# Kernel optimization log

Measured on AMD Instinct MI355X. Metric: run time of the kernel, lower is better.

## Reference

```python
import jax, jax.numpy as jnp
import numpy as np

K = 16  # matches init kwarg k


def setup_inputs() -> dict:
    key = jax.random.key(0)
    point_cloud = jax.random.normal(key, (4, 64, 4096), dtype=jnp.float32)
    return {"point_cloud": point_cloud}


def reference(point_cloud):
    B, dims, N = point_cloud.shape
    xt = jnp.transpose(point_cloud, (0, 2, 1))  # (B, N, dims)
    # pairwise euclidean distances (cdist, p=2)
    sq = jnp.sum(xt * xt, axis=-1)  # (B, N)
    d2 = sq[:, :, None] + sq[:, None, :] - 2.0 * jnp.einsum('bnd,bmd->bnm', xt, xt)
    dist = jnp.sqrt(jnp.maximum(d2, 0.0))  # (B, N, N)
    # k+1 smallest distances; drop self (first) neighbor
    _, idx_o = jax.lax.top_k(-dist, K + 1)  # (B, N, K+1)
    idx = idx_o[:, :, 1:]  # (B, N, K)
    # gather neighbor features: neighbors[b,d,n,j] = point_cloud[b,d,idx[b,n,j]]
    neighbors = jax.vmap(lambda pc, i: pc[:, i])(point_cloud, idx)  # (B, dims, N, K)
    central = point_cloud[:, :, :, None]  # (B, dims, N, 1)
    edge_feature = jnp.concatenate(
        [jnp.broadcast_to(central, (B, dims, N, K)), neighbors - central], axis=1
    )  # (B, 2*dims, N, K)
    return edge_feature, idx.reshape(B, -1)
```

## Files before the change

kernel.cpp:

```cpp
#include <hip/hip_runtime.h>


#define BATCH 4
#define DIMS 64
#define NPTS 4096
#define KNN 16
#define NCHUNK 32
#define CHLEN 128
#define GSZ 16
#define RN (BATCH * NPTS)
#define MLANES 8
#define MCH (NCHUNK / MLANES)

typedef unsigned long long u64;
typedef unsigned int u32;

__device__ __forceinline__ double sentinel() {
    return __longlong_as_double(0x7FEFFFFFFFFFFFFFLL);
}

__global__ __launch_bounds__(256) void ef_sq_kernel(const float* __restrict__ pc,
                                                    float* __restrict__ sq) {
    int gid = blockIdx.x * 256 + threadIdx.x;
    int b = gid >> 12;
    int n = gid & (NPTS - 1);
    const float* p = pc + (size_t)b * DIMS * NPTS + n;
    float r[8];
#pragma unroll
    for (int j = 0; j < 8; ++j) {
        float v = p[(size_t)j * NPTS];
        r[j] = __fmul_rn(v, v);
    }
#pragma unroll
    for (int i = 8; i < DIMS; i += 8) {
#pragma unroll
        for (int j = 0; j < 8; ++j) {
            float v = p[(size_t)(i + j) * NPTS];
            r[j] = __fadd_rn(r[j], __fmul_rn(v, v));
        }
    }
    float t01 = __fadd_rn(r[0], r[1]);
    float t23 = __fadd_rn(r[2], r[3]);
    float t45 = __fadd_rn(r[4], r[5]);
    float t67 = __fadd_rn(r[6], r[7]);
    sq[gid] = __fadd_rn(__fadd_rn(t01, t23), __fadd_rn(t45, t67));
}

__global__ __launch_bounds__(256) void ef_transpose(const float* __restrict__ pc,
                                                    float* __restrict__ pcT) {
    __shared__ float smT[DIMS][65];
    int tid = threadIdx.x;
    int m0 = blockIdx.x * 64;
    int b = blockIdx.y;
    const float* pcb = pc + (size_t)b * DIMS * NPTS;
#pragma unroll
    for (int i = 0; i < 16; ++i) {
        int idx = i * 256 + tid;
        int d = idx >> 6;
        int m = idx & 63;
        smT[d][m] = pcb[(size_t)d * NPTS + m0 + m];
    }
    __syncthreads();
#pragma unroll
    for (int i = 0; i < 16; ++i) {
        int idx = i * 256 + tid;
        int m = idx >> 6;
        int d = idx & 63;
        pcT[((size_t)b * NPTS + m0 + m) * DIMS + d] = smT[d][m];
    }
}

__global__ __launch_bounds__(256, 3) void ef_knn_partial(const float* __restrict__ pc,
                                                         const float* __restrict__ sq,
                                                         u64* __restrict__ pKey) {
    __shared__ float tile[DIMS][CHLEN];
    __shared__ float tileSq[CHLEN];
    int tid = threadIdx.x;
    int r = blockIdx.x * 256 + tid;
    int c = blockIdx.y;
    int b = (blockIdx.x * 256) >> 12;
    int n = r & (NPTS - 1);
    int m0 = c * CHLEN;
    const float* pcb = pc + (size_t)b * DIMS * NPTS;

    float xr[DIMS];
#pragma unroll
    for (int d = 0; d < DIMS; ++d) xr[d] = pcb[(size_t)d * NPTS + n];
#pragma unroll
    for (int d = 0; d < DIMS; ++d) asm volatile("" : "+v"(xr[d]));
    float sqn = sq[r];

#pragma unroll
    for (int i = 0; i < 8; ++i) {
        int idx = tid + i * 256;
        int d = idx >> 5;
        int mq = idx & 31;
        float4 v = *(const float4*)(pcb + (size_t)d * NPTS + m0 + mq * 4);
        *(float4*)&tile[d][mq * 4] = v;
    }
    if (tid < CHLEN / 4)
        *(float4*)&tileSq[tid * 4] =
            *(const float4*)(sq + (size_t)b * NPTS + m0 + tid * 4);
    __syncthreads();

    double key[KNN];
#pragma unroll
    for (int j = 0; j < KNN; ++j) key[j] = sentinel();

#define CE(arr, i, jj) { double lo_ = fmin(arr[i], arr[jj]); double hi_ = fmax(arr[i], arr[jj]); arr[i] = lo_; arr[jj] = hi_; }

    for (int g = 0; g < CHLEN; g += GSZ) {
        float acc[GSZ];
#pragma unroll
        for (int j = 0; j < GSZ; ++j) acc[j] = 0.f;
#pragma unroll
        for (int d = 0; d < DIMS; ++d) {
            float xv = xr[d];
            float4 q0 = *(const float4*)&tile[d][g];
            float4 q1 = *(const float4*)&tile[d][g + 4];
            float4 q2 = *(const float4*)&tile[d][g + 8];
            float4 q3 = *(const float4*)&tile[d][g + 12];
            acc[0]  = fmaf(xv, q0.x, acc[0]);
            acc[1]  = fmaf(xv, q0.y, acc[1]);
            acc[2]  = fmaf(xv, q0.z, acc[2]);
            acc[3]  = fmaf(xv, q0.w, acc[3]);
            acc[4]  = fmaf(xv, q1.x, acc[4]);
            acc[5]  = fmaf(xv, q1.y, acc[5]);
            acc[6]  = fmaf(xv, q1.z, acc[6]);
            acc[7]  = fmaf(xv, q1.w, acc[7]);
            acc[8]  = fmaf(xv, q2.x, acc[8]);
            acc[9]  = fmaf(xv, q2.y, acc[9]);
            acc[10] = fmaf(xv, q2.z, acc[10]);
            acc[11] = fmaf(xv, q2.w, acc[11]);
            acc[12] = fmaf(xv, q3.x, acc[12]);
            acc[13] = fmaf(xv, q3.y, acc[13]);
            acc[14] = fmaf(xv, q3.z, acc[14]);
            acc[15] = fmaf(xv, q3.w, acc[15]);
        }
        float4 s0 = *(const float4*)&tileSq[g];
        float4 s1 = *(const float4*)&tileSq[g + 4];
        float4 s2 = *(const float4*)&tileSq[g + 8];
        float4 s3 = *(const float4*)&tileSq[g + 12];
        float sqv[GSZ] = {s0.x, s0.y, s0.z, s0.w, s1.x, s1.y, s1.z, s1.w,
                          s2.x, s2.y, s2.z, s2.w, s3.x, s3.y, s3.z, s3.w};
        double s[GSZ];
#pragma unroll
        for (int j = 0; j < GSZ; ++j) {
            int m = m0 + g + j;
            float t1 = __fadd_rn(sqn, sqv[j]);
            float d2 = __fsub_rn(t1, __fmul_rn(2.0f, acc[j]));
            float dist = __fsqrt_rn(fmaxf(d2, 0.f));
            u64 cu = ((u64)__float_as_uint(dist) << 32) | (u64)(u32)m;
            double cand = __longlong_as_double((long long)cu);
            s[j] = (m == n) ? sentinel() : cand;
        }
        CE(s, 0, 1) CE(s, 2, 3) CE(s, 4, 5) CE(s, 6, 7)
        CE(s, 0, 2) CE(s, 1, 3) CE(s, 4, 6) CE(s, 5, 7)
        CE(s, 1, 2) CE(s, 5, 6)
        CE(s, 0, 4) CE(s, 1, 5) CE(s, 2, 6) CE(s, 3, 7)
        CE(s, 2, 4) CE(s, 3, 5)
        CE(s, 1, 2) CE(s, 3, 4) CE(s, 5, 6)

        CE(s, 8, 9) CE(s, 10, 11) CE(s, 12, 13) CE(s, 14, 15)
        CE(s, 8, 10) CE(s, 9, 11) CE(s, 12, 14) CE(s, 13, 15)
        CE(s, 9, 10) CE(s, 13, 14)
        CE(s, 8, 12) CE(s, 9, 13) CE(s, 10, 14) CE(s, 11, 15)
        CE(s, 10, 12) CE(s, 11, 13)
        CE(s, 9, 10) CE(s, 11, 12) CE(s, 13, 14)

        CE(s, 0, 15) CE(s, 1, 14) CE(s, 2, 13) CE(s, 3, 12)
        CE(s, 4, 11) CE(s, 5, 10) CE(s, 6, 9)  CE(s, 7, 8)
        CE(s, 0, 4)  CE(s, 1, 5)  CE(s, 2, 6)  CE(s, 3, 7)
        CE(s, 8, 12) CE(s, 9, 13) CE(s, 10, 14) CE(s, 11, 15)
        CE(s, 0, 2)  CE(s, 1, 3)  CE(s, 4, 6)  CE(s, 5, 7)
        CE(s, 8, 10) CE(s, 9, 11) CE(s, 12, 14) CE(s, 13, 15)
        CE(s, 0, 1)  CE(s, 2, 3)  CE(s, 4, 5)  CE(s, 6, 7)
        CE(s, 8, 9)  CE(s, 10, 11) CE(s, 12, 13) CE(s, 14, 15)

#pragma unroll
        for (int j = 0; j < KNN; ++j) key[j] = fmin(key[j], s[KNN - 1 - j]);
#pragma unroll
        for (int st = 8; st >= 1; st >>= 1) {
#pragma unroll
            for (int j = 0; j < KNN; ++j) {
                if ((j & st) == 0) {
                    double a = key[j], d = key[j | st];
                    key[j] = fmin(a, d);
                    key[j | st] = fmax(a, d);
                }
            }
        }
    }
#undef CE

    u64* dst = pKey + ((size_t)c * RN + r) * KNN;
#pragma unroll
    for (int j = 0; j < KNN; ++j) dst[j] = (u64)__double_as_longlong(key[j]);
}

__global__ __launch_bounds__(256) void ef_knn_merge(const u64* __restrict__ pKey,
                                                    float* __restrict__ outIdxF) {
    int t = blockIdx.x * 256 + threadIdx.x;
    int r = t >> 3;
    int s = t & 7;
    double key[KNN];
    {
        const u64* src = pKey + ((size_t)(s * MCH) * RN + r) * KNN;
#pragma unroll
        for (int j = 0; j < KNN; ++j)
            key[j] = __longlong_as_double((long long)src[j]);
    }
    for (int ci = 1; ci < MCH; ++ci) {
        const u64* src = pKey + ((size_t)(s * MCH + ci) * RN + r) * KNN;
        double v[KNN];
#pragma unroll
        for (int j = 0; j < KNN; ++j)
            v[j] = __longlong_as_double((long long)src[j]);
#pragma unroll
        for (int j = 0; j < KNN; ++j) key[j] = fmin(key[j], v[KNN - 1 - j]);
#pragma unroll
        for (int st = 8; st >= 1; st >>= 1) {
#pragma unroll
            for (int j = 0; j < KNN; ++j) {
                if ((j & st) == 0) {
                    double a = key[j], d = key[j | st];
                    key[j] = fmin(a, d);
                    key[j | st] = fmax(a, d);
                }
            }
        }
    }
#pragma unroll
    for (int mask = 1; mask <= 4; mask <<= 1) {
        double oth[KNN];
#pragma unroll
        for (int j = 0; j < KNN; ++j) oth[j] = __shfl_xor(key[j], mask, 64);
#pragma unroll
        for (int j = 0; j < KNN; ++j) key[j] = fmin(key[j], oth[KNN - 1 - j]);
#pragma unroll
        for (int st = 8; st >= 1; st >>= 1) {
#pragma unroll
            for (int j = 0; j < KNN; ++j) {
                if ((j & st) == 0) {
                    double a = key[j], d = key[j | st];
                    key[j] = fmin(a, d);
                    key[j | st] = fmax(a, d);
                }
            }
        }
    }
    if (s == 0) {
        float* dstf = outIdxF + (size_t)r * KNN;
#pragma unroll
        for (int j = 0; j < KNN; ++j)
            dstf[j] = (float)(u32)((u64)__double_as_longlong(key[j]) & 0xFFFFFFFFu);
    }
}

__global__ __launch_bounds__(256) void ef_edge_kernelT(const float* __restrict__ pcT,
                                                       const float* __restrict__ idxF,
                                                       float* __restrict__ out) {
    int t = blockIdx.x * 256 + threadIdx.x;
    int b = t >> 14;
    int rem = t & 16383;
    int n = rem >> 2;
    int k0 = (rem & 3) * 4;
    float4 i4 = *(const float4*)(idxF + (((size_t)(b << 12) + n) << 4) + k0);
    int m0 = (int)i4.x, m1 = (int)i4.y, m2 = (int)i4.z, m3 = (int)i4.w;
    const float4* cr  = (const float4*)(pcT + ((size_t)(b << 12) + n)  * DIMS);
    const float4* nr0 = (const float4*)(pcT + ((size_t)(b << 12) + m0) * DIMS);
    const float4* nr1 = (const float4*)(pcT + ((size_t)(b << 12) + m1) * DIMS);
    const float4* nr2 = (const float4*)(pcT + ((size_t)(b << 12) + m2) * DIMS);
    const float4* nr3 = (const float4*)(pcT + ((size_t)(b << 12) + m3) * DIMS);
    float* ob = out + (size_t)b * 2 * DIMS * NPTS * KNN + (size_t)n * KNN + k0;
#pragma unroll
    for (int q = 0; q < DIMS / 4; ++q) {
        float4 c4 = cr[q];
        float4 a0 = nr0[q], a1 = nr1[q], a2 = nr2[q], a3 = nr3[q];
        float cv, nv0, nv1, nv2, nv3;
        float4 st;
        cv = c4.x; nv0 = a0.x; nv1 = a1.x; nv2 = a2.x; nv3 = a3.x;
        st = make_float4(cv, cv, cv, cv);
        *(float4*)(ob + (size_t)(4 * q + 0) * (NPTS * KNN)) = st;
        st = make_float4(nv0 - cv, nv1 - cv, nv2 - cv, nv3 - cv);
        *(float4*)(ob + (size_t)(DIMS + 4 * q + 0) * (NPTS * KNN)) = st;
        cv = c4.y; nv0 = a0.y; nv1 = a1.y; nv2 = a2.y; nv3 = a3.y;
        st = make_float4(cv, cv, cv, cv);
        *(float4*)(ob + (size_t)(4 * q + 1) * (NPTS * KNN)) = st;
        st = make_float4(nv0 - cv, nv1 - cv, nv2 - cv, nv3 - cv);
        *(float4*)(ob + (size_t)(DIMS + 4 * q + 1) * (NPTS * KNN)) = st;
        cv = c4.z; nv0 = a0.z; nv1 = a1.z; nv2 = a2.z; nv3 = a3.z;
        st = make_float4(cv, cv, cv, cv);
        *(float4*)(ob + (size_t)(4 * q + 2) * (NPTS * KNN)) = st;
        st = make_float4(nv0 - cv, nv1 - cv, nv2 - cv, nv3 - cv);
        *(float4*)(ob + (size_t)(DIMS + 4 * q + 2) * (NPTS * KNN)) = st;
        cv = c4.w; nv0 = a0.w; nv1 = a1.w; nv2 = a2.w; nv3 = a3.w;
        st = make_float4(cv, cv, cv, cv);
        *(float4*)(ob + (size_t)(4 * q + 3) * (NPTS * KNN)) = st;
        st = make_float4(nv0 - cv, nv1 - cv, nv2 - cv, nv3 - cv);
        *(float4*)(ob + (size_t)(DIMS + 4 * q + 3) * (NPTS * KNN)) = st;
    }
}

__global__ __launch_bounds__(256) void ef_edge_kernel(const float* __restrict__ pc,
                                                      const float* __restrict__ idxF,
                                                      float* __restrict__ out) {
    int gid = blockIdx.x * 256 + threadIdx.x;
    int b = gid >> 16;
    int nk = gid & 65535;
    int n = nk >> 4;
    int m = (int)idxF[gid];
    const float* pcb = pc + (size_t)b * DIMS * NPTS;
    float* ob = out + (size_t)b * 2 * DIMS * NPTS * KNN;
#pragma unroll
    for (int d = 0; d < DIMS; ++d) {
        float cv = pcb[(size_t)d * NPTS + n];
        float nv = pcb[(size_t)d * NPTS + m];
        ob[(size_t)d * (NPTS * KNN) + nk] = cv;
        ob[(size_t)(DIMS + d) * (NPTS * KNN) + nk] = nv - cv;
    }
}

extern "C" void kernel_launch(void* const* d_in, const int* in_sizes, int n_in,
                              void* d_out, int out_size, void* d_ws, size_t ws_size,
                              hipStream_t stream) {
    const float* pc = (const float*)d_in[0];
    float* out = (float*)d_out;

    u64* pKey = (u64*)d_out;
    float* sq = out + 16777216;
    float* outIdxF = out + (size_t)BATCH * 2 * DIMS * NPTS * KNN;
    float* pcT = (float*)d_ws;
    bool useT = ws_size >= (size_t)BATCH * NPTS * DIMS * sizeof(float);

    ef_sq_kernel<<<(BATCH * NPTS) / 256, 256, 0, stream>>>(pc, sq);
    if (useT)
        ef_transpose<<<dim3(NPTS / 64, BATCH), 256, 0, stream>>>(pc, pcT);
    ef_knn_partial<<<dim3((BATCH * NPTS) / 256, NCHUNK), 256, 0, stream>>>(pc, sq, pKey);
    ef_knn_merge<<<(BATCH * NPTS * MLANES) / 256, 256, 0, stream>>>(pKey, outIdxF);
    if (useT)
        ef_edge_kernelT<<<(BATCH * NPTS * KNN / 4) / 256, 256, 0, stream>>>(pcT, outIdxF, out);
    else
        ef_edge_kernel<<<(BATCH * NPTS * KNN) / 256, 256, 0, stream>>>(pc, outIdxF, out);
}
```

Baseline: 325.1 us.

## Use packed FMA and 8-wide candidate groups in KNN partial distance loop

Replaces the scalar FMA inner product with v_pk_fma_f32 inline assembly on duplicated x values, processing two candidates per instruction. The candidate group shrinks from 16 to 8, so each sorted group of 8 is merged into the top-16 by a bitonic step on the upper half only, dropping the 16-wide sort network. This aims to halve FMA issue count and cut sorting work per candidate. In exchange it doubles the number of merge passes per chunk and doubles register use for the x vector, which may lower occupancy.

```diff
diff --git a/kernel.cpp b/kernel.cpp
--- a/kernel.cpp
+++ b/kernel.cpp
@@ -7,13 +7,15 @@
 #define KNN 16
 #define NCHUNK 32
 #define CHLEN 128
-#define GSZ 16
+#define GSZ 8
 #define RN (BATCH * NPTS)
 #define MLANES 8
 #define MCH (NCHUNK / MLANES)
 
 typedef unsigned long long u64;
 typedef unsigned int u32;
+typedef float f32x2 __attribute__((ext_vector_type(2)));
+typedef float f32x4 __attribute__((ext_vector_type(4)));
 
 __device__ __forceinline__ double sentinel() {
     return __longlong_as_double(0x7FEFFFFFFFFFFFFFLL);
@@ -83,11 +85,12 @@
     int m0 = c * CHLEN;
     const float* pcb = pc + (size_t)b * DIMS * NPTS;
 
-    float xr[DIMS];
-#pragma unroll
-    for (int d = 0; d < DIMS; ++d) xr[d] = pcb[(size_t)d * NPTS + n];
-#pragma unroll
-    for (int d = 0; d < DIMS; ++d) asm volatile("" : "+v"(xr[d]));
+    f32x2 xrp[DIMS];
+#pragma unroll
+    for (int d = 0; d < DIMS; ++d) {
+        float v = pcb[(size_t)d * NPTS + n];
+        xrp[d] = (f32x2){v, v};
+    }
     float sqn = sq[r];
 
 #pragma unroll
@@ -108,47 +111,36 @@
     for (int j = 0; j < KNN; ++j) key[j] = sentinel();
 
 #define CE(arr, i, jj) { double lo_ = fmin(arr[i], arr[jj]); double hi_ = fmax(arr[i], arr[jj]); arr[i] = lo_; arr[jj] = hi_; }
+#define PKFMA(accv, xv, cv) asm("v_pk_fma_f32 %0, %1, %2, %0" : "+v"(accv) : "v"(xv), "v"(cv))
 
     for (int g = 0; g < CHLEN; g += GSZ) {
-        float acc[GSZ];
-#pragma unroll
-        for (int j = 0; j < GSZ; ++j) acc[j] = 0.f;
+        f32x2 accp[4];
+#pragma unroll
+        for (int j = 0; j < 4; ++j) accp[j] = (f32x2){0.f, 0.f};
 #pragma unroll
         for (int d = 0; d < DIMS; ++d) {
-            float xv = xr[d];
-            float4 q0 = *(const float4*)&tile[d][g];
-            float4 q1 = *(const float4*)&tile[d][g + 4];
-            float4 q2 = *(const float4*)&tile[d][g + 8];
-            float4 q3 = *(const float4*)&tile[d][g + 12];
-            acc[0]  = fmaf(xv, q0.x, acc[0]);
-            acc[1]  = fmaf(xv, q0.y, acc[1]);
-            acc[2]  = fmaf(xv, q0.z, acc[2]);
-            acc[3]  = fmaf(xv, q0.w, acc[3]);
-            acc[4]  = fmaf(xv, q1.x, acc[4]);
-            acc[5]  = fmaf(xv, q1.y, acc[5]);
-            acc[6]  = fmaf(xv, q1.z, acc[6]);
-            acc[7]  = fmaf(xv, q1.w, acc[7]);
-            acc[8]  = fmaf(xv, q2.x, acc[8]);
-            acc[9]  = fmaf(xv, q2.y, acc[9]);
-            acc[10] = fmaf(xv, q2.z, acc[10]);
-            acc[11] = fmaf(xv, q2.w, acc[11]);
-            acc[12] = fmaf(xv, q3.x, acc[12]);
-            acc[13] = fmaf(xv, q3.y, acc[13]);
-            acc[14] = fmaf(xv, q3.z, acc[14]);
-            acc[15] = fmaf(xv, q3.w, acc[15]);
-        }
-        float4 s0 = *(const float4*)&tileSq[g];
-        float4 s1 = *(const float4*)&tileSq[g + 4];
-        float4 s2 = *(const float4*)&tileSq[g + 8];
-        float4 s3 = *(const float4*)&tileSq[g + 12];
-        float sqv[GSZ] = {s0.x, s0.y, s0.z, s0.w, s1.x, s1.y, s1.z, s1.w,
-                          s2.x, s2.y, s2.z, s2.w, s3.x, s3.y, s3.z, s3.w};
+            f32x4 q0 = *(const f32x4*)&tile[d][g];
+            f32x4 q1 = *(const f32x4*)&tile[d][g + 4];
+            f32x2 c0 = __builtin_shufflevector(q0, q0, 0, 1);
+            f32x2 c1 = __builtin_shufflevector(q0, q0, 2, 3);
+            f32x2 c2 = __builtin_shufflevector(q1, q1, 0, 1);
+            f32x2 c3 = __builtin_shufflevector(q1, q1, 2, 3);
+            PKFMA(accp[0], xrp[d], c0);
+            PKFMA(accp[1], xrp[d], c1);
+            PKFMA(accp[2], xrp[d], c2);
+            PKFMA(accp[3], xrp[d], c3);
+        }
+        float4 sq_lo = *(const float4*)&tileSq[g];
+        float4 sq_hi = *(const float4*)&tileSq[g + 4];
+        float sqv[GSZ] = {sq_lo.x, sq_lo.y, sq_lo.z, sq_lo.w,
+                          sq_hi.x, sq_hi.y, sq_hi.z, sq_hi.w};
         double s[GSZ];
 #pragma unroll
         for (int j = 0; j < GSZ; ++j) {
             int m = m0 + g + j;
+            float a = accp[j / 2][j % 2];
             float t1 = __fadd_rn(sqn, sqv[j]);
-            float d2 = __fsub_rn(t1, __fmul_rn(2.0f, acc[j]));
+            float d2 = __fsub_rn(t1, __fmul_rn(2.0f, a));
             float dist = __fsqrt_rn(fmaxf(d2, 0.f));
             u64 cu = ((u64)__float_as_uint(dist) << 32) | (u64)(u32)m;
             double cand = __longlong_as_double((long long)cu);
@@ -160,25 +152,8 @@
         CE(s, 0, 4) CE(s, 1, 5) CE(s, 2, 6) CE(s, 3, 7)
         CE(s, 2, 4) CE(s, 3, 5)
         CE(s, 1, 2) CE(s, 3, 4) CE(s, 5, 6)
-
-        CE(s, 8, 9) CE(s, 10, 11) CE(s, 12, 13) CE(s, 14, 15)
-        CE(s, 8, 10) CE(s, 9, 11) CE(s, 12, 14) CE(s, 13, 15)
-        CE(s, 9, 10) CE(s, 13, 14)
-        CE(s, 8, 12) CE(s, 9, 13) CE(s, 10, 14) CE(s, 11, 15)
-        CE(s, 10, 12) CE(s, 11, 13)
-        CE(s, 9, 10) CE(s, 11, 12) CE(s, 13, 14)
-
-        CE(s, 0, 15) CE(s, 1, 14) CE(s, 2, 13) CE(s, 3, 12)
-        CE(s, 4, 11) CE(s, 5, 10) CE(s, 6, 9)  CE(s, 7, 8)
-        CE(s, 0, 4)  CE(s, 1, 5)  CE(s, 2, 6)  CE(s, 3, 7)
-        CE(s, 8, 12) CE(s, 9, 13) CE(s, 10, 14) CE(s, 11, 15)
-        CE(s, 0, 2)  CE(s, 1, 3)  CE(s, 4, 6)  CE(s, 5, 7)
-        CE(s, 8, 10) CE(s, 9, 11) CE(s, 12, 14) CE(s, 13, 15)
-        CE(s, 0, 1)  CE(s, 2, 3)  CE(s, 4, 5)  CE(s, 6, 7)
-        CE(s, 8, 9)  CE(s, 10, 11) CE(s, 12, 13) CE(s, 14, 15)
-
-#pragma unroll
-        for (int j = 0; j < KNN; ++j) key[j] = fmin(key[j], s[KNN - 1 - j]);
+#pragma unroll
+        for (int j = 8; j < 16; ++j) key[j] = fmin(key[j], s[15 - j]);
 #pragma unroll
         for (int st = 8; st >= 1; st >>= 1) {
 #pragma unroll
@@ -192,6 +167,7 @@
         }
     }
 #undef CE
+#undef PKFMA
 
     u64* dst = pKey + ((size_t)c * RN + r) * KNN;
 #pragma unroll
```

After: 437.0 us. 1.34x slower.
